# Kernel tuning notes

Measured on AMD Instinct MI355X. Metric: run time of the kernel, lower is better.

## Reference

```python
import jax, jax.numpy as jnp
import numpy as np
from jax.scipy.special import logsumexp

S = 4          # num_residual_streams
D = 1024       # dim
B, T = 2, 4096
SINKHORN_ITERS = 10
TAU = 0.05


def rmsnorm(x, gamma):
    # F.normalize(x, dim=-1) * sqrt(dim) * (gamma + 1)
    norm = jnp.sqrt(jnp.sum(x * x, axis=-1, keepdims=True))
    scale = jnp.asarray(x.shape[-1], x.dtype) ** 0.5
    return x / jnp.maximum(norm, 1e-12) * scale * (gamma + 1.0)


def sinkhorn_log(logits, num_iters=SINKHORN_ITERS, tau=TAU):
    Z = logits / tau                      # (..., n, n)
    u = jnp.zeros(Z.shape[:-1], Z.dtype)  # (..., n)
    v = jnp.zeros_like(u)
    for _ in range(num_iters):
        u = -logsumexp(Z + v[..., None, :], axis=-1)
        v = -logsumexp(Z + u[..., :, None], axis=-2)
    return jnp.exp(Z + u[..., :, None] + v[..., None, :])


def setup_inputs() -> dict:
    key = jax.random.key(0)
    ks = jax.random.split(key, 8)
    residuals = jax.random.normal(ks[0], (B, T, S, D), dtype=jnp.float32)
    gamma = jnp.zeros((S * D,), dtype=jnp.float32)             # RMSNorm gamma init
    w_res = 0.02 * jax.random.normal(ks[1], (S * S, S * D), dtype=jnp.float32)
    w_pre = 0.02 * jax.random.normal(ks[2], (S, S * D), dtype=jnp.float32)
    w_post = 0.02 * jax.random.normal(ks[3], (S, S * D), dtype=jnp.float32)
    beta_res = jnp.full((S, S), -8.0, dtype=jnp.float32).at[jnp.arange(S), jnp.arange(S)].set(0.0)
    beta_pre = jnp.full((S,), -8.0, dtype=jnp.float32).at[0].set(0.0)  # layer_index=0
    beta_post = jnp.zeros((S,), dtype=jnp.float32)
    alpha_res = jnp.asarray(0.01, dtype=jnp.float32)
    alpha_pre = jnp.asarray(0.01, dtype=jnp.float32)
    alpha_post = jnp.asarray(0.01, dtype=jnp.float32)
    return dict(residuals=residuals, gamma=gamma, w_res=w_res, w_pre=w_pre,
                w_post=w_post, beta_res=beta_res, beta_pre=beta_pre,
                beta_post=beta_post, alpha_res=alpha_res, alpha_pre=alpha_pre,
                alpha_post=alpha_post)


def reference(residuals, gamma, w_res, w_pre, w_post, beta_res, beta_pre,
              beta_post, alpha_res, alpha_pre, alpha_post):
    b, t, s, d = residuals.shape
    h = residuals.reshape(b, t, s * d)
    normed = rmsnorm(h, gamma)                                  # (b,t,s*d)
    # dynamic H logits: static beta + alpha * linear(normed)
    res_logits = beta_res + alpha_res * jnp.einsum('btk,ek->bte', normed, w_res).reshape(b, t, s, s)
    H_res = sinkhorn_log(res_logits)                            # (b,t,s,s) doubly stochastic
    H_pre = jax.nn.softmax(beta_pre + alpha_pre * jnp.einsum('btk,sk->bts', normed, w_pre), axis=-1)
    H_post = 2.0 * jax.nn.sigmoid(beta_post + alpha_post * jnp.einsum('btk,sk->bts', normed, w_post))
    branch_in = jnp.einsum('bts,btsd->btd', H_pre, residuals)   # stream pooling -> branch input
    branch_out = branch_in                                      # identity branch
    mixed = jnp.einsum('btij,btjd->btid', H_res, residuals)     # stream remixing
    out = mixed + H_post[..., None] * branch_out[:, :, None, :]
    return out
```

## Files before the change

### kernel.cpp

```cpp
#include <hip/hip_runtime.h>
#include <math.h>

#define TOK_PER_BLK 2
#define THREADS 256
#define NROWS 24
#define PCOL 68
#define TAU_INV 20.0f

typedef _Float16 half2_t __attribute__((ext_vector_type(2)));

__global__ void fold_gamma(const float* __restrict__ w_res,
                           const float* __restrict__ w_pre,
                           const float* __restrict__ w_post,
                           const float* __restrict__ gamma,
                           unsigned int* __restrict__ wf) {
    const int idx = blockIdx.x * THREADS + threadIdx.x;
    const int row = idx >> 11;
    const int j   = idx & 2047;
    const int o   = j >> 2;
    const int pp  = j & 3;
    const int t   = o & 255;
    const int quad = pp >> 1;
    int base;
    if (o < 256) base = (quad == 0) ? (4 * t)        : (1024 + 4 * t);
    else         base = (quad == 0) ? (2048 + 4 * t) : (3072 + 4 * t);
    const int k0 = base + 2 * (pp & 1);

    const float* src = (row < 16) ? (w_res + ((size_t)row << 12))
                     : (row < 20) ? (w_pre + ((size_t)(row - 16) << 12))
                                  : (w_post + ((size_t)(row - 20) << 12));
    float v0 = src[k0]     * (1.0f + gamma[k0]);
    float v1 = src[k0 + 1] * (1.0f + gamma[k0 + 1]);
    union { _Float16 h[2]; unsigned int u; } cvt;
    cvt.h[0] = (_Float16)v0;
    cvt.h[1] = (_Float16)v1;
    wf[idx] = cvt.u;
}

__global__ __launch_bounds__(THREADS, 2)
void hc_fused(const float* __restrict__ resid,
              const unsigned int* __restrict__ wf,
              const float* __restrict__ beta_res,
              const float* __restrict__ beta_pre,
              const float* __restrict__ beta_post,
              const float* __restrict__ p_alpha_res,
              const float* __restrict__ p_alpha_pre,
              const float* __restrict__ p_alpha_post,
              float* __restrict__ out)
{
    __shared__ __align__(16) float sh_part[NROWS * TOK_PER_BLK][PCOL];
    __shared__ __align__(16) float sh_ssqp[TOK_PER_BLK][PCOL];
    __shared__ float sh_raw[TOK_PER_BLK][NROWS];
    __shared__ float sh_ssq[TOK_PER_BLK];
    __shared__ float sh_M[TOK_PER_BLK][16];

    const int tid  = threadIdx.x;
    const int wave = tid >> 6;
    const int lane = tid & 63;
    const long tok0 = (long)blockIdx.x * TOK_PER_BLK;

    const float4* hp = (const float4*)resid + tok0 * 1024;
    half2_t xh[TOK_PER_BLK][8];
    #pragma unroll
    for (int m = 0; m < TOK_PER_BLK; ++m) {
        float4 pf[4];
        #pragma unroll
        for (int q = 0; q < 4; ++q)
            pf[q] = hp[m * 1024 + q * 256 + tid];
        float s = 0.f;
        #pragma unroll
        for (int q = 0; q < 4; ++q) {
            float4 v = pf[q];
            s += v.x * v.x + v.y * v.y + v.z * v.z + v.w * v.w;
            xh[m][2 * q]     = half2_t{(_Float16)v.x, (_Float16)v.y};
            xh[m][2 * q + 1] = half2_t{(_Float16)v.z, (_Float16)v.w};
        }
        s += __shfl_xor(s, 16, 64);
        s += __shfl_xor(s, 32, 64);
        if (lane < 16) sh_ssqp[m][wave * 16 + lane] = s;
    }

    const uint4* wp = (const uint4*)wf;

    auto load_row = [&](int e, uint4 (&w)[2]) {
        const uint4* wr = wp + ((size_t)e << 9);
        w[0] = wr[tid];
        w[1] = wr[256 + tid];
    };
#define H2(u) __builtin_bit_cast(half2_t, (u))
    auto comp_row = [&](int e, const uint4 (&W)[2]) {
        #pragma unroll
        for (int m = 0; m < TOK_PER_BLK; ++m) {
            float a = 0.f;
            a = __builtin_amdgcn_fdot2(H2(W[0].x), xh[m][0], a, false);
            a = __builtin_amdgcn_fdot2(H2(W[0].y), xh[m][1], a, false);
            a = __builtin_amdgcn_fdot2(H2(W[0].z), xh[m][2], a, false);
            a = __builtin_amdgcn_fdot2(H2(W[0].w), xh[m][3], a, false);
            a = __builtin_amdgcn_fdot2(H2(W[1].x), xh[m][4], a, false);
            a = __builtin_amdgcn_fdot2(H2(W[1].y), xh[m][5], a, false);
            a = __builtin_amdgcn_fdot2(H2(W[1].z), xh[m][6], a, false);
            a = __builtin_amdgcn_fdot2(H2(W[1].w), xh[m][7], a, false);
            a += __shfl_xor(a, 16, 64);
            a += __shfl_xor(a, 32, 64);
            if (lane < 16) sh_part[e * TOK_PER_BLK + m][wave * 16 + lane] = a;
        }
    };
#undef H2

    uint4 wA[2], wB[2], wC[2];
    load_row(0, wA);
    load_row(1, wB);
    #pragma unroll 1
    for (int c = 0; c < 8; ++c) {
        load_row(3 * c + 2, wC);
        comp_row(3 * c, wA);
        if (3 * c + 3 < NROWS) load_row(3 * c + 3, wA);
        comp_row(3 * c + 1, wB);
        if (3 * c + 4 < NROWS) load_row(3 * c + 4, wB);
        comp_row(3 * c + 2, wC);
    }
    __syncthreads();

    if (tid < NROWS * TOK_PER_BLK) {
        const float4* src = (const float4*)&sh_part[tid][0];
        float4 s4 = src[0];
        #pragma unroll
        for (int j = 1; j < 16; ++j) {
            float4 v = src[j];
            s4.x += v.x; s4.y += v.y; s4.z += v.z; s4.w += v.w;
        }
        sh_raw[tid & (TOK_PER_BLK - 1)][tid >> 1] = s4.x + s4.y + s4.z + s4.w;
    } else if (tid < NROWS * TOK_PER_BLK + TOK_PER_BLK) {
        const int m = tid - NROWS * TOK_PER_BLK;
        const float4* src = (const float4*)&sh_ssqp[m][0];
        float4 s4 = src[0];
        #pragma unroll
        for (int j = 1; j < 16; ++j) {
            float4 v = src[j];
            s4.x += v.x; s4.y += v.y; s4.z += v.z; s4.w += v.w;
        }
        sh_ssq[m] = s4.x + s4.y + s4.z + s4.w;
    }
    __syncthreads();

    if (wave < TOK_PER_BLK) {
        const int m   = wave;
        const int idx = lane & 15;
        const int jj  = idx & 3;

        float ss    = sh_ssq[m];
        float scale = 64.0f / fmaxf(sqrtf(ss), 1e-12f);

        const float a_res  = p_alpha_res[0];
        const float a_pre  = p_alpha_pre[0];
        const float a_post = p_alpha_post[0];

        float Z = (beta_res[idx] + a_res * scale * sh_raw[m][idx]) * TAU_INV;
        float u = 0.f, v = 0.f;
        #pragma unroll 1
        for (int it = 0; it < 10; ++it) {
            float t  = Z + v;
            float mx = t;
            mx = fmaxf(mx, __shfl_xor(mx, 1, 64));
            mx = fmaxf(mx, __shfl_xor(mx, 2, 64));
            float sm = __expf(t - mx);
            sm += __shfl_xor(sm, 1, 64);
            sm += __shfl_xor(sm, 2, 64);
            u = -(mx + __logf(sm));
            t  = Z + u;
            mx = t;
            mx = fmaxf(mx, __shfl_xor(mx, 4, 64));
            mx = fmaxf(mx, __shfl_xor(mx, 8, 64));
            sm = __expf(t - mx);
            sm += __shfl_xor(sm, 4, 64);
            sm += __shfl_xor(sm, 8, 64);
            v = -(mx + __logf(sm));
        }
        float P = __expf(Z + u + v);

        float lpre = beta_pre[jj] + a_pre * scale * sh_raw[m][16 + jj];
        float mxp = lpre;
        mxp = fmaxf(mxp, __shfl_xor(mxp, 1, 64));
        mxp = fmaxf(mxp, __shfl_xor(mxp, 2, 64));
        float ep = __expf(lpre - mxp);
        float sp = ep;
        sp += __shfl_xor(sp, 1, 64);
        sp += __shfl_xor(sp, 2, 64);
        float hpre = ep / sp;
        float lpost = beta_post[jj] + a_post * scale * sh_raw[m][20 + jj];
        float hpost = 2.0f / (1.0f + __expf(-lpost));

        float hpost_i = __shfl(hpost, idx >> 2, 64);
        float Mv = P + hpost_i * hpre;
        if (lane < 16) sh_M[m][idx] = Mv;
    }
    __syncthreads();

    #pragma unroll
    for (int m = 0; m < TOK_PER_BLK; ++m) {
        float Mv[16];
        #pragma unroll
        for (int k = 0; k < 16; ++k) Mv[k] = sh_M[m][k];

        float xm[16];
        #pragma unroll
        for (int q = 0; q < 4; ++q) {
            xm[4*q + 0] = (float)xh[m][2*q][0];
            xm[4*q + 1] = (float)xh[m][2*q][1];
            xm[4*q + 2] = (float)xh[m][2*q + 1][0];
            xm[4*q + 3] = (float)xh[m][2*q + 1][1];
        }

        float4* op = (float4*)out + (tok0 + m) * 1024;
        #pragma unroll
        for (int i = 0; i < 4; ++i) {
            float4 o;
            o.x = Mv[i*4+0]*xm[0] + Mv[i*4+1]*xm[4]  + Mv[i*4+2]*xm[8]  + Mv[i*4+3]*xm[12];
            o.y = Mv[i*4+0]*xm[1] + Mv[i*4+1]*xm[5]  + Mv[i*4+2]*xm[9]  + Mv[i*4+3]*xm[13];
            o.z = Mv[i*4+0]*xm[2] + Mv[i*4+1]*xm[6]  + Mv[i*4+2]*xm[10] + Mv[i*4+3]*xm[14];
            o.w = Mv[i*4+0]*xm[3] + Mv[i*4+1]*xm[7]  + Mv[i*4+2]*xm[11] + Mv[i*4+3]*xm[15];
            op[i * 256 + tid] = o;
        }
    }
}

extern "C" void kernel_launch(void* const* d_in, const int* in_sizes, int n_in,
                              void* d_out, int out_size, void* d_ws, size_t ws_size,
                              hipStream_t stream) {
    const float* resid      = (const float*)d_in[0];
    const float* gamma      = (const float*)d_in[1];
    const float* w_res      = (const float*)d_in[2];
    const float* w_pre      = (const float*)d_in[3];
    const float* w_post     = (const float*)d_in[4];
    const float* beta_res   = (const float*)d_in[5];
    const float* beta_pre   = (const float*)d_in[6];
    const float* beta_post  = (const float*)d_in[7];
    const float* alpha_res  = (const float*)d_in[8];
    const float* alpha_pre  = (const float*)d_in[9];
    const float* alpha_post = (const float*)d_in[10];
    float* out = (float*)d_out;

    unsigned int* wf = (unsigned int*)d_ws;
    (void)ws_size;

    fold_gamma<<<NROWS * 2048 / THREADS, THREADS, 0, stream>>>(
        w_res, w_pre, w_post, gamma, wf);

    const int ntok = in_sizes[0] / 4096;
    const int grid = ntok / TOK_PER_BLK;

    hc_fused<<<grid, THREADS, 0, stream>>>(resid, wf, beta_res, beta_pre,
                                           beta_post, alpha_res, alpha_pre,
                                           alpha_post, out);
}
```

Baseline: 283.1 us.

## Split fused kernel into dots, sinkhorn, and apply kernels

Breaks the single fused kernel into three launches: a projection/sum-of-squares kernel now processing four tokens per block that writes raw logits to global workspace, a Sinkhorn kernel packing four tokens per wave, and a per-token apply kernel that re-reads the residuals in fp32. The aim is to stop most waves idling during the serial Sinkhorn phase and to amortise weight loads over more tokens. The cost is a second full read of the residual tensor, extra launches, and global round-trips for the intermediates. The apply step now uses fp32 residuals instead of the fp16 copies held in registers.

New measurement: 298.7 us. 1.06x slower.

```diff
diff --git a/kernel.cpp b/kernel.cpp
--- a/kernel.cpp
+++ b/kernel.cpp
@@ -1,7 +1,7 @@
 #include <hip/hip_runtime.h>
 #include <math.h>
 
-#define TOK_PER_BLK 2
+#define TOK_PER_BLK 4
 #define THREADS 256
 #define NROWS 24
 #define PCOL 68
@@ -38,21 +38,12 @@
 }
 
 __global__ __launch_bounds__(THREADS, 2)
-void hc_fused(const float* __restrict__ resid,
-              const unsigned int* __restrict__ wf,
-              const float* __restrict__ beta_res,
-              const float* __restrict__ beta_pre,
-              const float* __restrict__ beta_post,
-              const float* __restrict__ p_alpha_res,
-              const float* __restrict__ p_alpha_pre,
-              const float* __restrict__ p_alpha_post,
-              float* __restrict__ out)
+void hc_dots(const float* __restrict__ resid,
+             const unsigned int* __restrict__ wf,
+             float* __restrict__ g_raw)
 {
     __shared__ __align__(16) float sh_part[NROWS * TOK_PER_BLK][PCOL];
     __shared__ __align__(16) float sh_ssqp[TOK_PER_BLK][PCOL];
-    __shared__ float sh_raw[TOK_PER_BLK][NROWS];
-    __shared__ float sh_ssq[TOK_PER_BLK];
-    __shared__ float sh_M[TOK_PER_BLK][16];
 
     const int tid  = threadIdx.x;
     const int wave = tid >> 6;
@@ -122,14 +113,15 @@
     __syncthreads();
 
     if (tid < NROWS * TOK_PER_BLK) {
-        const float4* src = (const float4*)&sh_part[tid][0];
+        const int e = tid >> 2, m = tid & 3;
+        const float4* src = (const float4*)&sh_part[e * TOK_PER_BLK + m][0];
         float4 s4 = src[0];
         #pragma unroll
         for (int j = 1; j < 16; ++j) {
             float4 v = src[j];
             s4.x += v.x; s4.y += v.y; s4.z += v.z; s4.w += v.w;
         }
-        sh_raw[tid & (TOK_PER_BLK - 1)][tid >> 1] = s4.x + s4.y + s4.z + s4.w;
+        g_raw[(tok0 + m) * 32 + e] = s4.x + s4.y + s4.z + s4.w;
     } else if (tid < NROWS * TOK_PER_BLK + TOK_PER_BLK) {
         const int m = tid - NROWS * TOK_PER_BLK;
         const float4* src = (const float4*)&sh_ssqp[m][0];
@@ -139,88 +131,101 @@
             float4 v = src[j];
             s4.x += v.x; s4.y += v.y; s4.z += v.z; s4.w += v.w;
         }
-        sh_ssq[m] = s4.x + s4.y + s4.z + s4.w;
-    }
+        g_raw[(tok0 + m) * 32 + 24] = s4.x + s4.y + s4.z + s4.w;
+    }
+}
+
+__global__ void hc_sinkhorn(const float* __restrict__ g_raw,
+                            const float* __restrict__ beta_res,
+                            const float* __restrict__ beta_pre,
+                            const float* __restrict__ beta_post,
+                            const float* __restrict__ p_alpha_res,
+                            const float* __restrict__ p_alpha_pre,
+                            const float* __restrict__ p_alpha_post,
+                            float* __restrict__ g_M)
+{
+    const int tid  = threadIdx.x;
+    const int wave = tid >> 6;
+    const int lane = tid & 63;
+    const int grp  = lane >> 4;
+    const int idx  = lane & 15;
+    const int jj   = idx & 3;
+    const long t   = (long)blockIdx.x * 16 + wave * 4 + grp;
+
+    const float* rp = g_raw + t * 32;
+    float ss    = rp[24];
+    float scale = 64.0f / fmaxf(sqrtf(ss), 1e-12f);
+
+    const float a_res  = p_alpha_res[0];
+    const float a_pre  = p_alpha_pre[0];
+    const float a_post = p_alpha_post[0];
+
+    float Z = (beta_res[idx] + a_res * scale * rp[idx]) * TAU_INV;
+    float u = 0.f, v = 0.f;
+    #pragma unroll 1
+    for (int it = 0; it < 10; ++it) {
+        float tv = Z + v;
+        float mx = tv;
+        mx = fmaxf(mx, __shfl_xor(mx, 1, 64));
+        mx = fmaxf(mx, __shfl_xor(mx, 2, 64));
+        float sm = __expf(tv - mx);
+        sm += __shfl_xor(sm, 1, 64);
+        sm += __shfl_xor(sm, 2, 64);
+        u = -(mx + __logf(sm));
+        tv = Z + u;
+        mx = tv;
+        mx = fmaxf(mx, __shfl_xor(mx, 4, 64));
+        mx = fmaxf(mx, __shfl_xor(mx, 8, 64));
+        sm = __expf(tv - mx);
+        sm += __shfl_xor(sm, 4, 64);
+        sm += __shfl_xor(sm, 8, 64);
+        v = -(mx + __logf(sm));
+    }
+    float P = __expf(Z + u + v);
+
+    float lpre = beta_pre[jj] + a_pre * scale * rp[16 + jj];
+    float mxp = lpre;
+    mxp = fmaxf(mxp, __shfl_xor(mxp, 1, 64));
+    mxp = fmaxf(mxp, __shfl_xor(mxp, 2, 64));
+    float ep = __expf(lpre - mxp);
+    float sp = ep;
+    sp += __shfl_xor(sp, 1, 64);
+    sp += __shfl_xor(sp, 2, 64);
+    float hpre = ep / sp;
+    float lpost = beta_post[jj] + a_post * scale * rp[20 + jj];
+    float hpost = 2.0f / (1.0f + __expf(-lpost));
+
+    float hpost_i = __shfl(hpost, (lane & 48) | (idx >> 2), 64);
+    g_M[t * 16 + idx] = P + hpost_i * hpre;
+}
+
+__global__ void hc_apply(const float* __restrict__ resid,
+                         const float* __restrict__ g_M,
+                         float* __restrict__ out)
+{
+    __shared__ float sh_M[16];
+    const int tid = threadIdx.x;
+    const long t  = blockIdx.x;
+
+    if (tid < 16) sh_M[tid] = g_M[t * 16 + tid];
     __syncthreads();
 
-    if (wave < TOK_PER_BLK) {
-        const int m   = wave;
-        const int idx = lane & 15;
-        const int jj  = idx & 3;
-
-        float ss    = sh_ssq[m];
-        float scale = 64.0f / fmaxf(sqrtf(ss), 1e-12f);
-
-        const float a_res  = p_alpha_res[0];
-        const float a_pre  = p_alpha_pre[0];
-        const float a_post = p_alpha_post[0];
-
-        float Z = (beta_res[idx] + a_res * scale * sh_raw[m][idx]) * TAU_INV;
-        float u = 0.f, v = 0.f;
-        #pragma unroll 1
-        for (int it = 0; it < 10; ++it) {
-            float t  = Z + v;
-            float mx = t;
-            mx = fmaxf(mx, __shfl_xor(mx, 1, 64));
-            mx = fmaxf(mx, __shfl_xor(mx, 2, 64));
-            float sm = __expf(t - mx);
-            sm += __shfl_xor(sm, 1, 64);
-            sm += __shfl_xor(sm, 2, 64);
-            u = -(mx + __logf(sm));
-            t  = Z + u;
-            mx = t;
-            mx = fmaxf(mx, __shfl_xor(mx, 4, 64));
-            mx = fmaxf(mx, __shfl_xor(mx, 8, 64));
-            sm = __expf(t - mx);
-            sm += __shfl_xor(sm, 4, 64);
-            sm += __shfl_xor(sm, 8, 64);
-            v = -(mx + __logf(sm));
-        }
-        float P = __expf(Z + u + v);
-
-        float lpre = beta_pre[jj] + a_pre * scale * sh_raw[m][16 + jj];
-        float mxp = lpre;
-        mxp = fmaxf(mxp, __shfl_xor(mxp, 1, 64));
-        mxp = fmaxf(mxp, __shfl_xor(mxp, 2, 64));
-        float ep = __expf(lpre - mxp);
-        float sp = ep;
-        sp += __shfl_xor(sp, 1, 64);
-        sp += __shfl_xor(sp, 2, 64);
-        float hpre = ep / sp;
-        float lpost = beta_post[jj] + a_post * scale * sh_raw[m][20 + jj];
-        float hpost = 2.0f / (1.0f + __expf(-lpost));
-
-        float hpost_i = __shfl(hpost, idx >> 2, 64);
-        float Mv = P + hpost_i * hpre;
-        if (lane < 16) sh_M[m][idx] = Mv;
-    }
-    __syncthreads();
-
+    const float4* xp = (const float4*)resid + t * 1024;
+    float4 x0 = xp[tid], x1 = xp[256 + tid], x2 = xp[512 + tid], x3 = xp[768 + tid];
+
+    float Mv[16];
     #pragma unroll
-    for (int m = 0; m < TOK_PER_BLK; ++m) {
-        float Mv[16];
-        #pragma unroll
-        for (int k = 0; k < 16; ++k) Mv[k] = sh_M[m][k];
-
-        float xm[16];
-        #pragma unroll
-        for (int q = 0; q < 4; ++q) {
-            xm[4*q + 0] = (float)xh[m][2*q][0];
-            xm[4*q + 1] = (float)xh[m][2*q][1];
-            xm[4*q + 2] = (float)xh[m][2*q + 1][0];
-            xm[4*q + 3] = (float)xh[m][2*q + 1][1];
-        }
-
-        float4* op = (float4*)out + (tok0 + m) * 1024;
-        #pragma unroll
-        for (int i = 0; i < 4; ++i) {
-            float4 o;
-            o.x = Mv[i*4+0]*xm[0] + Mv[i*4+1]*xm[4]  + Mv[i*4+2]*xm[8]  + Mv[i*4+3]*xm[12];
-            o.y = Mv[i*4+0]*xm[1] + Mv[i*4+1]*xm[5]  + Mv[i*4+2]*xm[9]  + Mv[i*4+3]*xm[13];
-            o.z = Mv[i*4+0]*xm[2] + Mv[i*4+1]*xm[6]  + Mv[i*4+2]*xm[10] + Mv[i*4+3]*xm[14];
-            o.w = Mv[i*4+0]*xm[3] + Mv[i*4+1]*xm[7]  + Mv[i*4+2]*xm[11] + Mv[i*4+3]*xm[15];
-            op[i * 256 + tid] = o;
-        }
+    for (int k = 0; k < 16; ++k) Mv[k] = sh_M[k];
+
+    float4* op = (float4*)out + t * 1024;
+    #pragma unroll
+    for (int i = 0; i < 4; ++i) {
+        float4 o;
+        o.x = Mv[i*4+0]*x0.x + Mv[i*4+1]*x1.x + Mv[i*4+2]*x2.x + Mv[i*4+3]*x3.x;
+        o.y = Mv[i*4+0]*x0.y + Mv[i*4+1]*x1.y + Mv[i*4+2]*x2.y + Mv[i*4+3]*x3.y;
+        o.z = Mv[i*4+0]*x0.z + Mv[i*4+1]*x1.z + Mv[i*4+2]*x2.z + Mv[i*4+3]*x3.z;
+        o.w = Mv[i*4+0]*x0.w + Mv[i*4+1]*x1.w + Mv[i*4+2]*x2.w + Mv[i*4+3]*x3.w;
+        op[i * 256 + tid] = o;
     }
 }
 
@@ -240,16 +245,22 @@
     const float* alpha_post = (const float*)d_in[10];
     float* out = (float*)d_out;
 
-    unsigned int* wf = (unsigned int*)d_ws;
+    const int ntok = in_sizes[0] / 4096;
+
+    char* ws = (char*)d_ws;
+    unsigned int* wf  = (unsigned int*)ws;
+    float* g_raw      = (float*)(ws + 192 * 1024);
+    float* g_M        = (float*)(ws + 192 * 1024 + (size_t)ntok * 32 * 4);
     (void)ws_size;
 
     fold_gamma<<<NROWS * 2048 / THREADS, THREADS, 0, stream>>>(
         w_res, w_pre, w_post, gamma, wf);
 
-    const int ntok = in_sizes[0] / 4096;
-    const int grid = ntok / TOK_PER_BLK;
-
-    hc_fused<<<grid, THREADS, 0, stream>>>(resid, wf, beta_res, beta_pre,
-                                           beta_post, alpha_res, alpha_pre,
-                                           alpha_post, out);
-}
+    hc_dots<<<ntok / TOK_PER_BLK, THREADS, 0, stream>>>(resid, wf, g_raw);
+
+    hc_sinkhorn<<<ntok / 16, THREADS, 0, stream>>>(
+        g_raw, beta_res, beta_pre, beta_post,
+        alpha_res, alpha_pre, alpha_post, g_M);
+
+    hc_apply<<<ntok, THREADS, 0, stream>>>(resid, g_M, out);
+}
```

## Replicate folded weights per block group, use nontemporal I/O, deepen weight prefetch

Applied to the files above, without the earlier changes.

The gamma-folded fp16 weight matrix is now written in 8 copies, and each block reads the copy picked by its block index. This spreads the many concurrent weight reads across different memory lines and channels instead of all blocks hammering one copy. Residual loads and output stores use nontemporal hints so the streamed activations do not evict the weights from cache. The weight prefetch pipeline also moves from 3 to 4 rows in flight. In exchange the fold kernel writes 8 times as much data, the workspace must be 8 times larger, and each row buffer adds register pressure.

Result: faster. 277.0 us (-2.2%).

```diff
diff --git a/kernel.cpp b/kernel.cpp
--- a/kernel.cpp
+++ b/kernel.cpp
@@ -6,8 +6,12 @@
 #define NROWS 24
 #define PCOL 68
 #define TAU_INV 20.0f
+#define WCOPY 8
+#define WROW_U32 2048
+#define WCOPY_U32 (NROWS * WROW_U32)
 
 typedef _Float16 half2_t __attribute__((ext_vector_type(2)));
+typedef float    f32x4  __attribute__((ext_vector_type(4)));
 
 __global__ void fold_gamma(const float* __restrict__ w_res,
                            const float* __restrict__ w_pre,
@@ -34,7 +38,9 @@
     union { _Float16 h[2]; unsigned int u; } cvt;
     cvt.h[0] = (_Float16)v0;
     cvt.h[1] = (_Float16)v1;
-    wf[idx] = cvt.u;
+    #pragma unroll
+    for (int c = 0; c < WCOPY; ++c)
+        wf[(size_t)c * WCOPY_U32 + idx] = cvt.u;
 }
 
 __global__ __launch_bounds__(THREADS, 2)
@@ -59,18 +65,18 @@
     const int lane = tid & 63;
     const long tok0 = (long)blockIdx.x * TOK_PER_BLK;
 
-    const float4* hp = (const float4*)resid + tok0 * 1024;
+    const f32x4* hp = (const f32x4*)resid + tok0 * 1024;
     half2_t xh[TOK_PER_BLK][8];
     #pragma unroll
     for (int m = 0; m < TOK_PER_BLK; ++m) {
-        float4 pf[4];
+        f32x4 pf[4];
         #pragma unroll
         for (int q = 0; q < 4; ++q)
-            pf[q] = hp[m * 1024 + q * 256 + tid];
+            pf[q] = __builtin_nontemporal_load(&hp[m * 1024 + q * 256 + tid]);
         float s = 0.f;
         #pragma unroll
         for (int q = 0; q < 4; ++q) {
-            float4 v = pf[q];
+            f32x4 v = pf[q];
             s += v.x * v.x + v.y * v.y + v.z * v.z + v.w * v.w;
             xh[m][2 * q]     = half2_t{(_Float16)v.x, (_Float16)v.y};
             xh[m][2 * q + 1] = half2_t{(_Float16)v.z, (_Float16)v.w};
@@ -80,7 +86,7 @@
         if (lane < 16) sh_ssqp[m][wave * 16 + lane] = s;
     }
 
-    const uint4* wp = (const uint4*)wf;
+    const uint4* wp = (const uint4*)(wf + (size_t)(blockIdx.x & (WCOPY - 1)) * WCOPY_U32);
 
     auto load_row = [&](int e, uint4 (&w)[2]) {
         const uint4* wr = wp + ((size_t)e << 9);
@@ -107,17 +113,21 @@
     };
 #undef H2
 
-    uint4 wA[2], wB[2], wC[2];
+    uint4 wA[2], wB[2], wC[2], wD[2];
     load_row(0, wA);
     load_row(1, wB);
+    load_row(2, wC);
+    load_row(3, wD);
     #pragma unroll 1
-    for (int c = 0; c < 8; ++c) {
-        load_row(3 * c + 2, wC);
-        comp_row(3 * c, wA);
-        if (3 * c + 3 < NROWS) load_row(3 * c + 3, wA);
-        comp_row(3 * c + 1, wB);
-        if (3 * c + 4 < NROWS) load_row(3 * c + 4, wB);
-        comp_row(3 * c + 2, wC);
+    for (int c = 0; c < 6; ++c) {
+        comp_row(4 * c + 0, wA);
+        if (4 * c + 4 < NROWS) load_row(4 * c + 4, wA);
+        comp_row(4 * c + 1, wB);
+        if (4 * c + 5 < NROWS) load_row(4 * c + 5, wB);
+        comp_row(4 * c + 2, wC);
+        if (4 * c + 6 < NROWS) load_row(4 * c + 6, wC);
+        comp_row(4 * c + 3, wD);
+        if (4 * c + 7 < NROWS) load_row(4 * c + 7, wD);
     }
     __syncthreads();
 
@@ -159,19 +169,19 @@
         float u = 0.f, v = 0.f;
         #pragma unroll 1
         for (int it = 0; it < 10; ++it) {
-            float t  = Z + v;
-            float mx = t;
+            float tv = Z + v;
+            float mx = tv;
             mx = fmaxf(mx, __shfl_xor(mx, 1, 64));
             mx = fmaxf(mx, __shfl_xor(mx, 2, 64));
-            float sm = __expf(t - mx);
+            float sm = __expf(tv - mx);
             sm += __shfl_xor(sm, 1, 64);
             sm += __shfl_xor(sm, 2, 64);
             u = -(mx + __logf(sm));
-            t  = Z + u;
-            mx = t;
+            tv = Z + u;
+            mx = tv;
             mx = fmaxf(mx, __shfl_xor(mx, 4, 64));
             mx = fmaxf(mx, __shfl_xor(mx, 8, 64));
-            sm = __expf(t - mx);
+            sm = __expf(tv - mx);
             sm += __shfl_xor(sm, 4, 64);
             sm += __shfl_xor(sm, 8, 64);
             v = -(mx + __logf(sm));
@@ -211,15 +221,15 @@
             xm[4*q + 3] = (float)xh[m][2*q + 1][1];
         }
 
-        float4* op = (float4*)out + (tok0 + m) * 1024;
+        f32x4* op = (f32x4*)out + (tok0 + m) * 1024;
         #pragma unroll
         for (int i = 0; i < 4; ++i) {
-            float4 o;
+            f32x4 o;
             o.x = Mv[i*4+0]*xm[0] + Mv[i*4+1]*xm[4]  + Mv[i*4+2]*xm[8]  + Mv[i*4+3]*xm[12];
             o.y = Mv[i*4+0]*xm[1] + Mv[i*4+1]*xm[5]  + Mv[i*4+2]*xm[9]  + Mv[i*4+3]*xm[13];
             o.z = Mv[i*4+0]*xm[2] + Mv[i*4+1]*xm[6]  + Mv[i*4+2]*xm[10] + Mv[i*4+3]*xm[14];
             o.w = Mv[i*4+0]*xm[3] + Mv[i*4+1]*xm[7]  + Mv[i*4+2]*xm[11] + Mv[i*4+3]*xm[15];
-            op[i * 256 + tid] = o;
+            __builtin_nontemporal_store(o, &op[i * 256 + tid]);
         }
     }
 }
```
